# Performance work log

Hardware: AMD Instinct MI355X
Metric: run time of the kernel (lower is better)

The kernel has to match this reference:

```python
import jax, jax.numpy as jnp
import numpy as np

B, T, N, H = 256, 128, 512, 128  # batch, timesteps, input_size (driving series), hidden


def setup_inputs() -> dict:
    key = jax.random.key(0)
    ks = jax.random.split(key, 7)
    p = lambda k, shape: (jax.random.normal(k, shape, dtype=jnp.float32) * 0.05)
    return {
        "X": jax.random.normal(ks[0], (B, T, N), dtype=jnp.float32),
        # attention linear: in_features = 2H + T, out_features = 1 (stored as a vector + scalar bias)
        "attn_w": p(ks[1], (2 * H + T,)),
        "attn_b": p(ks[2], ()),
        # LSTM cell params, PyTorch layout/gate order (i, f, g, o)
        "w_ih": p(ks[3], (4 * H, N)),
        "w_hh": p(ks[4], (4 * H, H)),
        "b_ih": p(ks[5], (4 * H,)),
        "b_hh": p(ks[6], (4 * H,)),
    }


def reference(X, attn_w, attn_b, w_ih, w_hh, b_ih, b_hh):
    Bn, Tn, Nn = X.shape
    Hh = w_hh.shape[1]
    # split the single attention weight row into the h / s / X-row pieces of the concat
    w_h, w_s, w_x = attn_w[:Hh], attn_w[Hh:2 * Hh], attn_w[2 * Hh:]
    Xp = jnp.swapaxes(X, 1, 2)            # [B, N, T]  (X.permute(0,2,1))
    x_score = Xp @ w_x                    # [B, N], time-invariant part of attention logits

    def step(carry, x_t):                 # x_t: [B, N] = X[:, t, :]
        h, c = carry
        # logits[b,i] = w_h.h[b] + w_s.c[b] + w_x.Xp[b,i] + b  (== Linear on the concat)
        score = x_score + (h @ w_h + c @ w_s + attn_b)[:, None]   # [B, N]
        alpha = jax.nn.softmax(score, axis=1)
        x_tilde = alpha * x_t                                      # [B, N]
        gates = x_tilde @ w_ih.T + h @ w_hh.T + b_ih + b_hh        # [B, 4H]
        i, f, g, o = jnp.split(gates, 4, axis=1)
        c_new = jax.nn.sigmoid(f) * c + jax.nn.sigmoid(i) * jnp.tanh(g)
        h_new = jax.nn.sigmoid(o) * jnp.tanh(c_new)
        return (h_new, c_new), (x_tilde, h_new)

    h0 = jnp.zeros((Bn, Hh), X.dtype)
    (_, _), (Xt, Xe) = jax.lax.scan(step, (h0, h0), jnp.swapaxes(X, 0, 1))
    # scan stacks along time -> [T, B, .]; return [B, T, .]
    return jnp.swapaxes(Xt, 0, 1), jnp.swapaxes(Xe, 0, 1)
```

## Files before the change

kernel.cpp:

```cpp
#include <hip/hip_runtime.h>
#include <hip/hip_bf16.h>

#define Bb 256
#define Tt 128
#define Nn 512
#define Hh 128

typedef __attribute__((ext_vector_type(4))) float floatx4;
typedef __attribute__((ext_vector_type(8))) short short8;
typedef _Float16 h2v_t __attribute__((ext_vector_type(2)));

__device__ __forceinline__ unsigned short f2bf(float f) {
  unsigned u = __float_as_uint(f);
  u += 0x7fffu + ((u >> 16) & 1u);
  return (unsigned short)(u >> 16);
}

__device__ __forceinline__ float sigmoid_fast(float x) {
  return __builtin_amdgcn_rcpf(1.f + __expf(-x));
}
__device__ __forceinline__ float tanh_fast(float x) {
  float e = __expf(2.f * x);
  return 1.f - 2.f * __builtin_amdgcn_rcpf(e + 1.f);
}

__device__ __forceinline__ void lds_barrier() {
  asm volatile("s_waitcnt lgkmcnt(0)" ::: "memory");
  __builtin_amdgcn_s_barrier();
  asm volatile("" ::: "memory");
}

__device__ __forceinline__ void async_load16(const void* g, void* lds) {
  __builtin_amdgcn_global_load_lds(
      (const __attribute__((address_space(1))) unsigned int*)g,
      (__attribute__((address_space(3))) unsigned int*)lds, 16, 0, 0);
}

#if __has_builtin(__builtin_amdgcn_fdot2)
#define FDOT2(a, b, c) __builtin_amdgcn_fdot2((a), (b), (c), false)
#else
__device__ __forceinline__ float fdot2_sw(h2v_t a, h2v_t b, float c) {
  return fmaf((float)a.x, (float)b.x, fmaf((float)a.y, (float)b.y, (c)));
}
#define FDOT2(a, b, c) fdot2_sw((a), (b), (c))
#endif

template <int CTRL>
__device__ __forceinline__ float qbcast(float x) {
#if __has_builtin(__builtin_amdgcn_update_dpp)
  return __uint_as_float((unsigned)__builtin_amdgcn_update_dpp(
      0, (int)__float_as_uint(x), CTRL, 0xf, 0xf, true));
#else
  return __shfl(x, (threadIdx.x & ~3) + (CTRL & 3), 64);
#endif
}

__global__ void prep_kernel(const float* __restrict__ w_ih,
                            const float* __restrict__ b_ih,
                            const float* __restrict__ b_hh,
                            unsigned short* __restrict__ wb,
                            float* __restrict__ bias) {
  int i = blockIdx.x * 256 + threadIdx.x;
  if (i < 4 * Hh * Nn) wb[i] = f2bf(w_ih[i]);
  if (i < 4 * Hh) bias[i] = b_ih[i] + b_hh[i];
}

__global__ __launch_bounds__(512) void alpha_kernel(const float* __restrict__ X,
                                                    const float* __restrict__ attn_w,
                                                    float* __restrict__ alpha) {
  int b = blockIdx.x;
  int tid = threadIdx.x;
  int c = tid & 127;
  int tp = tid >> 7;
  const float4* Xb = (const float4*)(X + (size_t)b * Tt * Nn) + c;
  const float* wx = attn_w + 2 * Hh;

  float4 acc = {0.f, 0.f, 0.f, 0.f};
#pragma unroll 8
  for (int tt = 0; tt < 32; ++tt) {
    int t = tp * 32 + tt;
    float4 x = Xb[(size_t)t * 128];
    float w = wx[t];
    acc.x = fmaf(x.x, w, acc.x);
    acc.y = fmaf(x.y, w, acc.y);
    acc.z = fmaf(x.z, w, acc.z);
    acc.w = fmaf(x.w, w, acc.w);
  }

  __shared__ float4 s4[512];
  __shared__ float sred[128];
  s4[tid] = acc;
  __syncthreads();

  float4 sc = {0.f, 0.f, 0.f, 0.f};
  if (tid < 128) {
    float4 a = s4[tid], b2 = s4[tid + 128], c2 = s4[tid + 256], d = s4[tid + 384];
    sc.x = a.x + b2.x + c2.x + d.x;
    sc.y = a.y + b2.y + c2.y + d.y;
    sc.z = a.z + b2.z + c2.z + d.z;
    sc.w = a.w + b2.w + c2.w + d.w;
    sred[tid] = fmaxf(fmaxf(sc.x, sc.y), fmaxf(sc.z, sc.w));
  }
  __syncthreads();
  for (int s = 64; s > 0; s >>= 1) {
    if (tid < s) sred[tid] = fmaxf(sred[tid], sred[tid + s]);
    __syncthreads();
  }
  float m = sred[0];
  __syncthreads();

  float4 e4 = {0.f, 0.f, 0.f, 0.f};
  if (tid < 128) {
    e4.x = __expf(sc.x - m);
    e4.y = __expf(sc.y - m);
    e4.z = __expf(sc.z - m);
    e4.w = __expf(sc.w - m);
    sred[tid] = e4.x + e4.y + e4.z + e4.w;
  }
  __syncthreads();
  for (int s = 64; s > 0; s >>= 1) {
    if (tid < s) sred[tid] += sred[tid + s];
    __syncthreads();
  }
  float inv = 1.f / sred[0];
  if (tid < 128) {
    float4 out;
    out.x = e4.x * inv; out.y = e4.y * inv; out.z = e4.z * inv; out.w = e4.w * inv;
    ((float4*)(alpha + (size_t)b * Nn))[tid] = out;
  }
}

__global__ __launch_bounds__(256) void scale_kernel(const float* __restrict__ X,
                                                    const float* __restrict__ alpha,
                                                    float* __restrict__ Xt,
                                                    unsigned short* __restrict__ xtb) {
  size_t i = (size_t)blockIdx.x * 256 + threadIdx.x;
  size_t e = i * 4;
  int n = (int)(e & (Nn - 1));
  int brow = (int)(e >> 9);
  int b = brow >> 7;
  float4 x = ((const float4*)X)[i];
  float4 a = *(const float4*)(alpha + (size_t)b * Nn + n);
  float4 y;
  y.x = x.x * a.x; y.y = x.y * a.y; y.z = x.z * a.z; y.w = x.w * a.w;
  ((float4*)Xt)[i] = y;
  ushort4 u;
  u.x = f2bf(y.x); u.y = f2bf(y.y); u.z = f2bf(y.z); u.w = f2bf(y.w);
  ((ushort4*)xtb)[i] = u;
}

#define GBK 64

__global__ __launch_bounds__(256) void gemm_bt(const unsigned short* __restrict__ A,
                                               const unsigned short* __restrict__ Bw,
                                               const float* __restrict__ bias,
                                               float* __restrict__ C) {
  __shared__ __align__(16) unsigned short As[128 * 64];
  __shared__ __align__(16) unsigned short Bs[128 * 64];
  const int K = 512, NO = 512;
  int tid = threadIdx.x;
  int lane = tid & 63;
  int wave = tid >> 6;
  int wm = wave & 1, wn = wave >> 1;
  int l15 = lane & 15;
  int quad = lane >> 4;
  int mtile = blockIdx.x, ntile = blockIdx.y;

  floatx4 acc[4][4];
#pragma unroll
  for (int i = 0; i < 4; ++i)
#pragma unroll
    for (int j = 0; j < 4; ++j) acc[i][j] = (floatx4){0.f, 0.f, 0.f, 0.f};

  int lr = lane >> 3;
  int lc = (lane & 7) ^ lr;
  const size_t lane_goff = (size_t)lr * K + lc * 8;
  const size_t abase = (size_t)mtile * 128 * K + lane_goff;
  const size_t bbase = (size_t)ntile * 128 * K + lane_goff;
  int sw = (quad ^ (l15 & 7)) * 8;

  for (int kb = 0; kb < K; kb += GBK) {
#pragma unroll
    for (int slot = 0; slot < 4; ++slot) {
      int r0 = slot * 32 + wave * 8;
      async_load16(A + abase + (size_t)r0 * K + kb, &As[r0 * 64]);
      async_load16(Bw + bbase + (size_t)r0 * K + kb, &Bs[r0 * 64]);
    }
    __syncthreads();
#pragma unroll
    for (int kh = 0; kh < 2; ++kh) {
      int sc = sw ^ (kh * 32);
      short8 af[4], bf[4];
#pragma unroll
      for (int i = 0; i < 4; ++i)
        af[i] = *(const short8*)(&As[(wm * 64 + i * 16 + l15) * 64 + sc]);
#pragma unroll
      for (int j = 0; j < 4; ++j)
        bf[j] = *(const short8*)(&Bs[(wn * 64 + j * 16 + l15) * 64 + sc]);
#pragma unroll
      for (int i = 0; i < 4; ++i)
#pragma unroll
        for (int j = 0; j < 4; ++j)
          acc[i][j] = __builtin_amdgcn_mfma_f32_16x16x32_bf16(af[i], bf[j], acc[i][j], 0, 0, 0);
    }
    __syncthreads();
  }

  int m0 = mtile * 128 + wm * 64;
  int n0 = ntile * 128 + wn * 64;
#pragma unroll
  for (int j = 0; j < 4; ++j) {
    int col = n0 + j * 16 + l15;
    float bsum = bias[col];
#pragma unroll
    for (int i = 0; i < 4; ++i) {
      int row = m0 + i * 16 + quad * 4;
#pragma unroll
      for (int r = 0; r < 4; ++r)
        C[(size_t)(row + r) * NO + col] = acc[i][j][r] + bsum;
    }
  }
}

__global__ __launch_bounds__(512, 1) void lstm_kernel(const float* __restrict__ G,
                                                      const float* __restrict__ w_hh,
                                                      float* __restrict__ Xe) {
  int b = blockIdx.x;
  int tid = threadIdx.x;
  int u = tid >> 2;
  int f = tid & 3;

  h2v_t wreg[64];
  {
    const float4* wr = (const float4*)(w_hh + (size_t)(f * 128 + u) * 128);
#pragma unroll
    for (int i = 0; i < 32; ++i) {
      float4 v = wr[i];
      wreg[2 * i]     = (h2v_t){(_Float16)v.x, (_Float16)v.y};
      wreg[2 * i + 1] = (h2v_t){(_Float16)v.z, (_Float16)v.w};
    }
  }

  __shared__ __align__(16) unsigned short h2[2][128];
  if (tid < 128) h2[0][tid] = 0;
  __syncthreads();

  const float* Gb = G + (size_t)b * Tt * 512 + f * 128 + u;
  float* Xeb = Xe + (size_t)b * Tt * Hh;

  float gcur = Gb[0];
  float gnext = Gb[512];
  float c0 = 0.f;

  const float actm = (f == 2) ? 2.f : -1.f;
  const float fA   = (f == 2) ? -2.f : 1.f;
  const float fB   = (f == 2) ? 1.f : 0.f;

#define H2F(W) __builtin_bit_cast(h2v_t, (W))

  for (int t = 0; t < Tt; ++t) {
    int cur = t & 1;
    const uint4* hp = (const uint4*)(&h2[cur][0]);

    float g_this = gcur;
    gcur = gnext;
    if (t + 2 < Tt) gnext = Gb[(size_t)(t + 2) * 512];

    float a0 = g_this, a1 = 0.f;
#pragma unroll
    for (int ch = 0; ch < 4; ++ch) {
      uint4 r0 = hp[ch * 4 + 0], r1 = hp[ch * 4 + 1];
      uint4 r2 = hp[ch * 4 + 2], r3 = hp[ch * 4 + 3];
      const h2v_t* wk = &wreg[ch * 16];
      a0 = FDOT2(H2F(r0.x), wk[0],  a0);  a1 = FDOT2(H2F(r0.y), wk[1],  a1);
      a0 = FDOT2(H2F(r0.z), wk[2],  a0);  a1 = FDOT2(H2F(r0.w), wk[3],  a1);
      a0 = FDOT2(H2F(r1.x), wk[4],  a0);  a1 = FDOT2(H2F(r1.y), wk[5],  a1);
      a0 = FDOT2(H2F(r1.z), wk[6],  a0);  a1 = FDOT2(H2F(r1.w), wk[7],  a1);
      a0 = FDOT2(H2F(r2.x), wk[8],  a0);  a1 = FDOT2(H2F(r2.y), wk[9],  a1);
      a0 = FDOT2(H2F(r2.z), wk[10], a0);  a1 = FDOT2(H2F(r2.w), wk[11], a1);
      a0 = FDOT2(H2F(r3.x), wk[12], a0);  a1 = FDOT2(H2F(r3.y), wk[13], a1);
      a0 = FDOT2(H2F(r3.z), wk[14], a0);  a1 = FDOT2(H2F(r3.w), wk[15], a1);
    }
    float x = a0 + a1;

    float e = __expf(x * actm);
    float r = __builtin_amdgcn_rcpf(1.f + e);
    float val = fmaf(r, fA, fB);

    float gi = qbcast<0x00>(val);
    float gf = qbcast<0x55>(val);
    float gg = qbcast<0xAA>(val);
    float go = qbcast<0xFF>(val);

    c0 = fmaf(gf, c0, gi * gg);
    float hv = go * tanh_fast(c0);

    if (f == 0) h2[cur ^ 1][u] = __builtin_bit_cast(unsigned short, (_Float16)hv);
    if (f == 1) Xeb[(size_t)t * Hh + u] = hv;
    lds_barrier();
  }
#undef H2F
}

extern "C" void kernel_launch(void* const* d_in, const int* in_sizes, int n_in,
                              void* d_out, int out_size, void* d_ws, size_t ws_size,
                              hipStream_t stream) {
  const float* X      = (const float*)d_in[0];
  const float* attn_w = (const float*)d_in[1];
  const float* w_ih   = (const float*)d_in[3];
  const float* w_hh   = (const float*)d_in[4];
  const float* b_ih   = (const float*)d_in[5];
  const float* b_hh   = (const float*)d_in[6];

  float* Xt = (float*)d_out;
  float* Xe = (float*)d_out + (size_t)Bb * Tt * Nn;

  char* ws = (char*)d_ws;
  float*          alpha = (float*)(ws);
  float*          bias  = (float*)(ws + 524288);
  unsigned short* wb    = (unsigned short*)(ws + 526336);
  unsigned short* xtb   = (unsigned short*)(ws + 1050624);
  float*          G     = (float*)(ws + 34605056);

  prep_kernel<<<dim3(1024), dim3(256), 0, stream>>>(w_ih, b_ih, b_hh, wb, bias);
  alpha_kernel<<<dim3(Bb), dim3(512), 0, stream>>>(X, attn_w, alpha);
  scale_kernel<<<dim3(16384), dim3(256), 0, stream>>>(X, alpha, Xt, xtb);
  gemm_bt<<<dim3(256, 4), dim3(256), 0, stream>>>(xtb, wb, bias, G);
  lstm_kernel<<<dim3(Bb), dim3(512), 0, stream>>>(G, w_hh, Xe);
}
```

Before: 276.6 us.

## Distribute recurrent matvec across 16-lane rings with DPP rotate-accumulate

Reorganises the LSTM recurrent matvec so each 16-lane ring computes 16 gate rows cooperatively. Each lane loads only one 16-byte chunk of h from LDS instead of the whole 256-byte vector, and partial sums are passed around the ring with DPP row rotations. This removes most of the per-step LDS read traffic, which sits on the serial critical path. In exchange it adds 32 dependent DPP rotates per step, and the gate combine is rebuilt on rotates with a select.

Result: no change. 276.9 us (+0.1%).

```diff
diff --git a/kernel.cpp b/kernel.cpp
--- a/kernel.cpp
+++ b/kernel.cpp
@@ -45,14 +45,19 @@
 #define FDOT2(a, b, c) fdot2_sw((a), (b), (c))
 #endif
 
+#define ROT1 0x121
+#define ROT4 0x124
 template <int CTRL>
-__device__ __forceinline__ float qbcast(float x) {
+__device__ __forceinline__ int rot_i(int x) {
 #if __has_builtin(__builtin_amdgcn_update_dpp)
-  return __uint_as_float((unsigned)__builtin_amdgcn_update_dpp(
-      0, (int)__float_as_uint(x), CTRL, 0xf, 0xf, true));
+  return __builtin_amdgcn_update_dpp(0, x, CTRL, 0xf, 0xf, true);
 #else
-  return __shfl(x, (threadIdx.x & ~3) + (CTRL & 3), 64);
+  return __shfl(x, (threadIdx.x & ~15) + (((threadIdx.x & 15) + (CTRL & 15)) & 15), 64);
 #endif
+}
+template <int CTRL>
+__device__ __forceinline__ float rot_f(float x) {
+  return __uint_as_float((unsigned)rot_i<CTRL>((int)__float_as_uint(x)));
 }
 
 __global__ void prep_kernel(const float* __restrict__ w_ih,
@@ -227,25 +232,40 @@
                                                       float* __restrict__ Xe) {
   int b = blockIdx.x;
   int tid = threadIdx.x;
-  int u = tid >> 2;
-  int f = tid & 3;
+  int w = tid >> 6;
+  int l = tid & 63;
+  int ring = l >> 4;
+  int r = l & 15;
+  int f = r >> 2;
+  int usub = r & 3;
+  int ubase = w * 16 + ring * 4;
+  int unit = ubase + usub;
 
   h2v_t wreg[64];
   {
-    const float4* wr = (const float4*)(w_hh + (size_t)(f * 128 + u) * 128);
-#pragma unroll
-    for (int i = 0; i < 32; ++i) {
-      float4 v = wr[i];
-      wreg[2 * i]     = (h2v_t){(_Float16)v.x, (_Float16)v.y};
-      wreg[2 * i + 1] = (h2v_t){(_Float16)v.z, (_Float16)v.w};
-    }
-  }
+    int idx = r;
+#pragma unroll
+    for (int p = 0; p < 16; ++p) {
+      int j = idx;
+      const float* wr = w_hh + (size_t)((j >> 2) * 128 + ubase + (j & 3)) * 128 + r * 8;
+      float4 v0 = *(const float4*)(wr);
+      float4 v1 = *(const float4*)(wr + 4);
+      wreg[p * 4 + 0] = (h2v_t){(_Float16)v0.x, (_Float16)v0.y};
+      wreg[p * 4 + 1] = (h2v_t){(_Float16)v0.z, (_Float16)v0.w};
+      wreg[p * 4 + 2] = (h2v_t){(_Float16)v1.x, (_Float16)v1.y};
+      wreg[p * 4 + 3] = (h2v_t){(_Float16)v1.z, (_Float16)v1.w};
+      if (p < 15) idx = rot_i<ROT1>(idx);
+    }
+  }
+
+  int g1 = rot_i<ROT4>(f);
+  bool plus = (g1 == ((f + 1) & 3));
 
   __shared__ __align__(16) unsigned short h2[2][128];
   if (tid < 128) h2[0][tid] = 0;
   __syncthreads();
 
-  const float* Gb = G + (size_t)b * Tt * 512 + f * 128 + u;
+  const float* Gb = G + (size_t)b * Tt * 512 + f * 128 + unit;
   float* Xeb = Xe + (size_t)b * Tt * Hh;
 
   float gcur = Gb[0];
@@ -260,7 +280,7 @@
 
   for (int t = 0; t < Tt; ++t) {
     int cur = t & 1;
-    const uint4* hp = (const uint4*)(&h2[cur][0]);
+    uint4 hq = *(const uint4*)(&h2[cur][r * 8]);
 
     float g_this = gcur;
     gcur = gnext;
@@ -268,35 +288,31 @@
 
     float a0 = g_this, a1 = 0.f;
 #pragma unroll
-    for (int ch = 0; ch < 4; ++ch) {
-      uint4 r0 = hp[ch * 4 + 0], r1 = hp[ch * 4 + 1];
-      uint4 r2 = hp[ch * 4 + 2], r3 = hp[ch * 4 + 3];
-      const h2v_t* wk = &wreg[ch * 16];
-      a0 = FDOT2(H2F(r0.x), wk[0],  a0);  a1 = FDOT2(H2F(r0.y), wk[1],  a1);
-      a0 = FDOT2(H2F(r0.z), wk[2],  a0);  a1 = FDOT2(H2F(r0.w), wk[3],  a1);
-      a0 = FDOT2(H2F(r1.x), wk[4],  a0);  a1 = FDOT2(H2F(r1.y), wk[5],  a1);
-      a0 = FDOT2(H2F(r1.z), wk[6],  a0);  a1 = FDOT2(H2F(r1.w), wk[7],  a1);
-      a0 = FDOT2(H2F(r2.x), wk[8],  a0);  a1 = FDOT2(H2F(r2.y), wk[9],  a1);
-      a0 = FDOT2(H2F(r2.z), wk[10], a0);  a1 = FDOT2(H2F(r2.w), wk[11], a1);
-      a0 = FDOT2(H2F(r3.x), wk[12], a0);  a1 = FDOT2(H2F(r3.y), wk[13], a1);
-      a0 = FDOT2(H2F(r3.z), wk[14], a0);  a1 = FDOT2(H2F(r3.w), wk[15], a1);
+    for (int p = 0; p < 16; ++p) {
+      a0 = FDOT2(H2F(hq.x), wreg[p * 4 + 0], a0);
+      a0 = FDOT2(H2F(hq.y), wreg[p * 4 + 1], a0);
+      a1 = FDOT2(H2F(hq.z), wreg[p * 4 + 2], a1);
+      a1 = FDOT2(H2F(hq.w), wreg[p * 4 + 3], a1);
+      a0 = rot_f<ROT1>(a0);
+      a1 = rot_f<ROT1>(a1);
     }
     float x = a0 + a1;
 
     float e = __expf(x * actm);
-    float r = __builtin_amdgcn_rcpf(1.f + e);
-    float val = fmaf(r, fA, fB);
-
-    float gi = qbcast<0x00>(val);
-    float gf = qbcast<0x55>(val);
-    float gg = qbcast<0xAA>(val);
-    float go = qbcast<0xFF>(val);
-
-    c0 = fmaf(gf, c0, gi * gg);
-    float hv = go * tanh_fast(c0);
-
-    if (f == 0) h2[cur ^ 1][u] = __builtin_bit_cast(unsigned short, (_Float16)hv);
-    if (f == 1) Xeb[(size_t)t * Hh + u] = hv;
+    float val = fmaf(__builtin_amdgcn_rcpf(1.f + e), fA, fB);
+
+    float x1 = rot_f<ROT4>(val);
+    float x2 = rot_f<ROT4>(x1);
+    float x3 = rot_f<ROT4>(x2);
+    float gfv = plus ? x1 : x3;
+    float gov = plus ? x3 : x1;
+
+    if (f == 0) {
+      c0 = fmaf(gfv, c0, val * x2);
+      float hv = gov * tanh_fast(c0);
+      h2[cur ^ 1][unit] = __builtin_bit_cast(unsigned short, (_Float16)hv);
+      Xeb[(size_t)t * Hh + unit] = hv;
+    }
     lds_barrier();
   }
 #undef H2F
```
